# Kernel optimization log

Hardware: AMD Instinct MI355X
Metric: run time of the kernel (lower is better)

Reference implementation:

```python
import jax, jax.numpy as jnp
import numpy as np

SEQ_LEN, N_FEAT, EMB = 512, 8, 64
HID = 2 * EMB  # 128
BATCH = 512


def _lstm_layer(x, Wih, Whh, bih, bhh):
    """Single-layer LSTM, batch_first x: [B,T,F]. PyTorch gate order i,f,g,o.
    Returns (outputs [B,T,H], final hidden [B,H])."""
    B = x.shape[0]
    H = Whh.shape[1]
    # precompute input projections for all timesteps: [B,T,4H]
    xp = jnp.einsum('btf,gf->btg', x, Wih) + bih + bhh

    def step(carry, xt):
        h, c = carry
        gates = xt + h @ Whh.T  # [B,4H]
        i, f, g, o = jnp.split(gates, 4, axis=-1)
        i = jax.nn.sigmoid(i)
        f = jax.nn.sigmoid(f)
        g = jnp.tanh(g)
        o = jax.nn.sigmoid(o)
        c = f * c + i * g
        h = o * jnp.tanh(c)
        return (h, c), h

    h0 = jnp.zeros((B, H), dtype=x.dtype)
    c0 = jnp.zeros((B, H), dtype=x.dtype)
    (hT, _), hs = jax.lax.scan(step, (h0, c0), xp.transpose(1, 0, 2))
    return hs.transpose(1, 0, 2), hT


def setup_inputs() -> dict:
    key = jax.random.key(0)
    ks = jax.random.split(key, 13)
    inp = {"x": jax.random.normal(ks[0], (BATCH, SEQ_LEN, N_FEAT), dtype=jnp.float32)}

    def mk(k, shape, fan):
        s = 1.0 / np.sqrt(fan)
        return jax.random.uniform(k, shape, dtype=jnp.float32, minval=-s, maxval=s)

    # layer 1: in=N_FEAT, hid=HID
    inp["Wih1"] = mk(ks[1], (4 * HID, N_FEAT), HID)
    inp["Whh1"] = mk(ks[2], (4 * HID, HID), HID)
    inp["bih1"] = mk(ks[3], (4 * HID,), HID)
    inp["bhh1"] = mk(ks[4], (4 * HID,), HID)
    # layer 2: in=HID, hid=HID
    inp["Wih2"] = mk(ks[5], (4 * HID, HID), HID)
    inp["Whh2"] = mk(ks[6], (4 * HID, HID), HID)
    inp["bih2"] = mk(ks[7], (4 * HID,), HID)
    inp["bhh2"] = mk(ks[8], (4 * HID,), HID)
    # layer 3: in=HID, hid=EMB
    inp["Wih3"] = mk(ks[9], (4 * EMB, HID), EMB)
    inp["Whh3"] = mk(ks[10], (4 * EMB, EMB), EMB)
    inp["bih3"] = mk(ks[11], (4 * EMB,), EMB)
    inp["bhh3"] = mk(ks[12], (4 * EMB,), EMB)
    return inp


def reference(x, Wih1, Whh1, bih1, bhh1, Wih2, Whh2, bih2, bhh2, Wih3, Whh3, bih3, bhh3):
    B = x.shape[0]
    x = x.reshape(B, SEQ_LEN, N_FEAT)
    x, _ = _lstm_layer(x, Wih1, Whh1, bih1, bhh1)
    x, _ = _lstm_layer(x, Wih2, Whh2, bih2, bhh2)
    _, hT = _lstm_layer(x, Wih3, Whh3, bih3, bhh3)
    return hT  # [B, EMB]
```

## Files before the change

### kernel.cpp

```cpp
#include <hip/hip_runtime.h>


#define DEVI __device__ __forceinline__

typedef _Float16 h4 __attribute__((ext_vector_type(4)));
typedef _Float16 h8 __attribute__((ext_vector_type(8)));
typedef float f4 __attribute__((ext_vector_type(4)));

static constexpr int T_ = 512, TC_ = 16, NC_ = T_ / TC_, RC_ = 2;

DEVI float rcpf_(float x) { return __builtin_amdgcn_rcpf(x); }
DEVI float exp2f_(float x) { return __builtin_amdgcn_exp2f(x); }

DEVI h8 cvt8(const float* p) {
    const float4 a = *reinterpret_cast<const float4*>(p);
    const float4 b = *reinterpret_cast<const float4*>(p + 4);
    return h8{(_Float16)a.x, (_Float16)a.y, (_Float16)a.z, (_Float16)a.w,
              (_Float16)b.x, (_Float16)b.y, (_Float16)b.z, (_Float16)b.w};
}

DEVI void lds_barrier() {
    asm volatile("s_waitcnt lgkmcnt(0)\n\ts_barrier" ::: "memory");
}
DEVI int ld_flag(int* f) {
    return __hip_atomic_load(f, __ATOMIC_RELAXED, __HIP_MEMORY_SCOPE_AGENT);
}
DEVI void st_flag(int* f, int v) {
    __hip_atomic_store(f, v, __ATOMIC_RELAXED, __HIP_MEMORY_SCOPE_AGENT);
}

#define POINTWISE_PROLOG(ACC)                                                   \
    float e0[4], e1[4], e2[4], e3[4];                                           \
    _Pragma("unroll") for (int i = 0; i < 4; i++) {                             \
        e0[i] = exp2f_(ACC[0][i] * -1.44269504f);                               \
        e1[i] = exp2f_(ACC[1][i] * -1.44269504f);                               \
        e2[i] = exp2f_(ACC[2][i] * -2.88539008f);                               \
        e3[i] = exp2f_(ACC[3][i] * -1.44269504f); }

#define POINTWISE_CELL(i, C, HVAR)                                              \
    const float gi = rcpf_(1.f + e0[i]), gf = rcpf_(1.f + e1[i]);               \
    const float gg = 2.f * rcpf_(1.f + e2[i]) - 1.f, go = rcpf_(1.f + e3[i]);   \
    C[i] = gf * C[i] + gi * gg;                                                 \
    const float HVAR = go * (2.f * rcpf_(1.f + exp2f_(C[i] * -2.88539008f)) - 1.f);

DEVI void stage_L1(int tile, char* smem, const float* x, const float* Wih,
                   const float* Whh, const float* bih, const float* bhh,
                   _Float16* o1, int* c1, int* p1) {
    constexpr int H = 128, KT_H = 4, HP = H + 8;
    const int tid = threadIdx.x, lane = tid & 63, wv = tid >> 6;
    const int lr = lane & 15, lk = lane >> 4;
    const int b0 = tile * 16;
    const int jcol = wv * 16 + lr;
    _Float16 (*h_lds)[16][HP] = (_Float16 (*)[16][HP])smem;

    h8 wbh[4][KT_H], wbx[4];
    float bias[4];
#pragma unroll
    for (int q = 0; q < 4; q++) {
#pragma unroll
        for (int kt = 0; kt < KT_H; kt++)
            wbh[q][kt] = cvt8(Whh + (size_t)(q * H + jcol) * H + kt * 32 + lk * 8);
        wbx[q] = (lk == 0) ? cvt8(Wih + (size_t)(q * H + jcol) * 8) : h8{};
        bias[q] = bih[q * H + jcol] + bhh[q * H + jcol];
    }
    float c[4] = {0.f, 0.f, 0.f, 0.f};
    for (int i = tid; i < 2 * 16 * HP; i += 512) ((_Float16*)smem)[i] = (_Float16)0;
    __syncthreads();

    auto load_x = [&](int t, h8& xa) {
        xa = (lk == 0) ? cvt8(x + ((size_t)(b0 + lr) * T_ + t) * 8) : h8{};
    };
    h8 xa, xb;

#define L1_STEP(TT, CUR, XS) {                                                  \
    const int tt = (TT);                                                        \
    h8 ha[KT_H];                                                                \
    _Pragma("unroll") for (int kt = 0; kt < KT_H; kt++)                         \
        ha[kt] = *reinterpret_cast<const h8*>(&h_lds[CUR][lr][kt * 32 + lk * 8]); \
    f4 acc[4];                                                                  \
    _Pragma("unroll") for (int q = 0; q < 4; q++)                               \
        acc[q] = f4{bias[q], bias[q], bias[q], bias[q]};                        \
    _Pragma("unroll") for (int q = 0; q < 4; q++)                               \
        acc[q] = __builtin_amdgcn_mfma_f32_16x16x32_f16(XS, wbx[q], acc[q], 0, 0, 0); \
    _Pragma("unroll") for (int kt = 0; kt < KT_H; kt++)                         \
        _Pragma("unroll") for (int q = 0; q < 4; q++)                           \
            acc[q] = __builtin_amdgcn_mfma_f32_16x16x32_f16(ha[kt], wbh[q][kt], acc[q], 0, 0, 0); \
    if (tt + 2 < TC_) load_x(t0 + tt + 2, XS);                                  \
    POINTWISE_PROLOG(acc)                                                       \
    _Pragma("unroll") for (int i = 0; i < 4; i++) {                             \
        POINTWISE_CELL(i, c, h)                                                 \
        const int row = lk * 4 + i;                                             \
        h_lds[(CUR) ^ 1][row][jcol] = (_Float16)h;                              \
        o1[(((size_t)(tile * RC_ + slot) * TC_ + tt) * 16 + row) * 128 + jcol] = (_Float16)h; } }

    for (int ch = 0; ch < NC_; ch++) {
        const int slot = ch & (RC_ - 1);
        if (tid == 0) {
            while (ld_flag(c1) < ch - (RC_ - 1)) __builtin_amdgcn_s_sleep(8);
        }
        __syncthreads();
        const int t0 = ch * TC_;
        load_x(t0, xa); load_x(t0 + 1, xb);
        for (int tb = 0; tb < TC_ / 2; tb++) {
            L1_STEP(2 * tb, 0, xa) lds_barrier();
            L1_STEP(2 * tb + 1, 1, xb) lds_barrier();
        }
        asm volatile("s_waitcnt vmcnt(0)" ::: "memory");
        __syncthreads();
        if (tid == 0) { __threadfence(); st_flag(p1, ch + 1); }
    }
#undef L1_STEP
}

DEVI void stage_P2(int tile, const _Float16* o1, _Float16* xp, const float* Wih,
                   const float* bih, const float* bhh,
                   int* p1, int* c1, int* cx, int* px) {
    constexpr int H = 128;
    const int tid = threadIdx.x, lane = tid & 63, wv = tid >> 6;
    const int lr = lane & 15, lk = lane >> 4;
    const int jcol = wv * 16 + lr;

    h8 wbx[4][4];
    float pbias[4];
#pragma unroll
    for (int q = 0; q < 4; q++) {
#pragma unroll
        for (int kt = 0; kt < 4; kt++)
            wbx[q][kt] = cvt8(Wih + (size_t)(q * H + jcol) * 128 + kt * 32 + lk * 8);
        pbias[q] = bih[q * H + jcol] + bhh[q * H + jcol];
    }

    for (int ch = 0; ch < NC_; ch++) {
        const int slot = ch & (RC_ - 1);
        if (tid == 0) {
            while (ld_flag(p1) < ch + 1) __builtin_amdgcn_s_sleep(8);
            while (ld_flag(cx) < ch - (RC_ - 1)) __builtin_amdgcn_s_sleep(8);
            __threadfence();
        }
        __syncthreads();
        const size_t ib = (size_t)(tile * RC_ + slot) * TC_ * 2048;
        const size_t ob = (size_t)(tile * RC_ + slot) * TC_ * 8192;
#pragma unroll 4
        for (int t = 0; t < TC_; t++) {
            h8 af[4];
#pragma unroll
            for (int kt = 0; kt < 4; kt++)
                af[kt] = *reinterpret_cast<const h8*>(o1 + ib + (size_t)t * 2048 + lr * 128 + kt * 32 + lk * 8);
            f4 acc[4];
#pragma unroll
            for (int q = 0; q < 4; q++) acc[q] = f4{pbias[q], pbias[q], pbias[q], pbias[q]};
#pragma unroll
            for (int kt = 0; kt < 4; kt++)
#pragma unroll
                for (int q = 0; q < 4; q++)
                    acc[q] = __builtin_amdgcn_mfma_f32_16x16x32_f16(af[kt], wbx[q][kt], acc[q], 0, 0, 0);
#pragma unroll
            for (int q = 0; q < 4; q++) {
                const h4 o = h4{(_Float16)acc[q][0], (_Float16)acc[q][1],
                                (_Float16)acc[q][2], (_Float16)acc[q][3]};
                *reinterpret_cast<h4*>(xp + ob + (size_t)t * 8192 + (wv * 4 + q) * 256 + lane * 4) = o;
            }
        }
        asm volatile("s_waitcnt vmcnt(0)" ::: "memory");
        __syncthreads();
        if (tid == 0) { __threadfence(); st_flag(px, ch + 1); st_flag(c1, ch + 1); }
    }
}

DEVI void stage_L2(int tile, char* smem, const _Float16* xp, _Float16* O2,
                   const float* Whh, int* px, int* cx, int* p2) {
    constexpr int H = 128, KT_H = 4, HP = H + 8;
    const int tid = threadIdx.x, lane = tid & 63, wv = tid >> 6;
    const int lr = lane & 15, lk = lane >> 4;
    const int b0 = tile * 16;
    const int jcol = wv * 16 + lr;
    _Float16 (*h_lds)[16][HP] = (_Float16 (*)[16][HP])smem;

    h8 wbh[4][KT_H];
#pragma unroll
    for (int q = 0; q < 4; q++)
#pragma unroll
        for (int kt = 0; kt < KT_H; kt++)
            wbh[q][kt] = cvt8(Whh + (size_t)(q * H + jcol) * H + kt * 32 + lk * 8);

    float c[4] = {0.f, 0.f, 0.f, 0.f};
    for (int i = tid; i < 2 * 16 * HP; i += 512) ((_Float16*)smem)[i] = (_Float16)0;
    __syncthreads();

    h4 xqa[4], xqb[4];

#define LOAD_XP(SLOT, TTL, DST) {                                               \
    const size_t base = ((size_t)(tile * RC_ + (SLOT)) * TC_ + (TTL)) * 8192 + wv * 1024 + lane * 4; \
    _Pragma("unroll") for (int q = 0; q < 4; q++)                               \
        DST[q] = *reinterpret_cast<const h4*>(xp + base + q * 256); }

#define L2_STEP(TT, CUR, XQ) {                                                  \
    const int tt = (TT); const int t = t0 + tt;                                 \
    h8 ha[KT_H];                                                                \
    _Pragma("unroll") for (int kt = 0; kt < KT_H; kt++)                         \
        ha[kt] = *reinterpret_cast<const h8*>(&h_lds[CUR][lr][kt * 32 + lk * 8]); \
    f4 acc[4];                                                                  \
    _Pragma("unroll") for (int q = 0; q < 4; q++)                               \
        acc[q] = f4{(float)XQ[q][0], (float)XQ[q][1], (float)XQ[q][2], (float)XQ[q][3]}; \
    _Pragma("unroll") for (int kt = 0; kt < KT_H; kt++)                         \
        _Pragma("unroll") for (int q = 0; q < 4; q++)                           \
            acc[q] = __builtin_amdgcn_mfma_f32_16x16x32_f16(ha[kt], wbh[q][kt], acc[q], 0, 0, 0); \
    if (tt + 2 < TC_) LOAD_XP(slot, tt + 2, XQ)                                 \
    POINTWISE_PROLOG(acc)                                                       \
    _Pragma("unroll") for (int i = 0; i < 4; i++) {                             \
        POINTWISE_CELL(i, c, h)                                                 \
        const int row = lk * 4 + i;                                             \
        h_lds[(CUR) ^ 1][row][jcol] = (_Float16)h;                              \
        O2[((size_t)(b0 + row) * T_ + t) * 128 + jcol] = (_Float16)h; } }

    for (int ch = 0; ch < NC_; ch++) {
        const int slot = ch & (RC_ - 1);
        if (tid == 0) {
            while (ld_flag(px) < ch + 1) __builtin_amdgcn_s_sleep(8);
            __threadfence();
        }
        __syncthreads();
        const int t0 = ch * TC_;
        LOAD_XP(slot, 0, xqa)
        LOAD_XP(slot, 1, xqb)
        for (int tb = 0; tb < TC_ / 2; tb++) {
            L2_STEP(2 * tb, 0, xqa) lds_barrier();
            L2_STEP(2 * tb + 1, 1, xqb) lds_barrier();
        }
        asm volatile("s_waitcnt vmcnt(0)" ::: "memory");
        __syncthreads();
        if (tid == 0) { __threadfence(); st_flag(p2, ch + 1); st_flag(cx, ch + 1); }
    }
#undef L2_STEP
#undef LOAD_XP
}

DEVI void stage_L3(int tile, char* smem, const _Float16* O2, const float* Wih,
                   const float* Whh, const float* bih, const float* bhh,
                   float* out, int* p2) {
    constexpr int H = 64, KT_H = 2, KT_X = 4, HP = H + 8;
    const int tid = threadIdx.x, lane = tid & 63, wv = tid >> 6;
    const int lr = lane & 15, lk = lane >> 4;
    const int b0 = tile * 16;
    const bool act = (wv < 4);
    const int jcol = (wv & 3) * 16 + lr;
    _Float16 (*h_lds)[16][HP] = (_Float16 (*)[16][HP])smem;

    h8 wbh[4][KT_H], wbx[4][KT_X];
    float bias[4];
    if (act) {
#pragma unroll
        for (int q = 0; q < 4; q++) {
#pragma unroll
            for (int kt = 0; kt < KT_H; kt++)
                wbh[q][kt] = cvt8(Whh + (size_t)(q * H + jcol) * H + kt * 32 + lk * 8);
#pragma unroll
            for (int kt = 0; kt < KT_X; kt++)
                wbx[q][kt] = cvt8(Wih + (size_t)(q * H + jcol) * 128 + kt * 32 + lk * 8);
            bias[q] = bih[q * H + jcol] + bhh[q * H + jcol];
        }
    }
    float c[4] = {0.f, 0.f, 0.f, 0.f};
    for (int i = tid; i < 2 * 16 * HP; i += 512) ((_Float16*)smem)[i] = (_Float16)0;
    __syncthreads();

    auto load_x = [&](int t, h8* xa) {
#pragma unroll
        for (int kt = 0; kt < KT_X; kt++)
            xa[kt] = *reinterpret_cast<const h8*>(
                O2 + ((size_t)(b0 + lr) * T_ + t) * 128 + kt * 32 + lk * 8);
    };
    h8 xa[KT_X], xb[KT_X];

#define L3_STEP(TT, CUR, XS) {                                                  \
    const int tt = (TT); const int t = t0 + tt;                                 \
    if (act) {                                                                  \
        h8 ha[KT_H];                                                            \
        _Pragma("unroll") for (int kt = 0; kt < KT_H; kt++)                     \
            ha[kt] = *reinterpret_cast<const h8*>(&h_lds[CUR][lr][kt * 32 + lk * 8]); \
        f4 acc[4];                                                              \
        _Pragma("unroll") for (int q = 0; q < 4; q++)                           \
            acc[q] = f4{bias[q], bias[q], bias[q], bias[q]};                    \
        _Pragma("unroll") for (int kt = 0; kt < KT_X; kt++)                     \
            _Pragma("unroll") for (int q = 0; q < 4; q++)                       \
                acc[q] = __builtin_amdgcn_mfma_f32_16x16x32_f16(XS[kt], wbx[q][kt], acc[q], 0, 0, 0); \
        _Pragma("unroll") for (int kt = 0; kt < KT_H; kt++)                     \
            _Pragma("unroll") for (int q = 0; q < 4; q++)                       \
                acc[q] = __builtin_amdgcn_mfma_f32_16x16x32_f16(ha[kt], wbh[q][kt], acc[q], 0, 0, 0); \
        if (tt + 2 < TC_) load_x(t + 2, XS);                                    \
        POINTWISE_PROLOG(acc)                                                   \
        _Pragma("unroll") for (int i = 0; i < 4; i++) {                         \
            POINTWISE_CELL(i, c, h)                                             \
            const int row = lk * 4 + i;                                         \
            h_lds[(CUR) ^ 1][row][jcol] = (_Float16)h;                          \
            if (t == T_ - 1) out[(size_t)(b0 + row) * 64 + jcol] = h; } } }

    for (int ch = 0; ch < NC_; ch++) {
        if (tid == 0) {
            while (ld_flag(p2) < ch + 1) __builtin_amdgcn_s_sleep(8);
            __threadfence();
        }
        __syncthreads();
        const int t0 = ch * TC_;
        if (act) { load_x(t0, xa); load_x(t0 + 1, xb); }
        for (int tb = 0; tb < TC_ / 2; tb++) {
            L3_STEP(2 * tb, 0, xa) lds_barrier();
            L3_STEP(2 * tb + 1, 1, xb) lds_barrier();
        }
    }
#undef L3_STEP
}

__global__ __launch_bounds__(512, 1)
void mega_k(const float* __restrict__ x,
            const float* __restrict__ Wih1, const float* __restrict__ Whh1,
            const float* __restrict__ bih1, const float* __restrict__ bhh1,
            const float* __restrict__ Wih2, const float* __restrict__ Whh2,
            const float* __restrict__ bih2, const float* __restrict__ bhh2,
            const float* __restrict__ Wih3, const float* __restrict__ Whh3,
            const float* __restrict__ bih3, const float* __restrict__ bhh3,
            _Float16* __restrict__ o1ring, _Float16* __restrict__ xpring,
            _Float16* __restrict__ O2, float* __restrict__ out,
            int* __restrict__ flags) {
    extern __shared__ char smem[];
    const int bid = blockIdx.x;
    int* p1 = flags;
    int* c1 = flags + 32;
    int* px = flags + 64;
    int* cx = flags + 96;
    int* p2 = flags + 128;
    if (bid < 32) {
        stage_L1(bid, smem, x, Wih1, Whh1, bih1, bhh1, o1ring, c1 + bid, p1 + bid);
    } else if (bid < 64) {
        const int t = bid - 32;
        stage_P2(t, o1ring, xpring, Wih2, bih2, bhh2, p1 + t, c1 + t, cx + t, px + t);
    } else if (bid < 96) {
        const int t = bid - 64;
        stage_L2(t, smem, xpring, O2, Whh2, px + t, cx + t, p2 + t);
    } else {
        const int t = bid - 96;
        stage_L3(t, smem, O2, Wih3, Whh3, bih3, bhh3, out, p2 + t);
    }
}

__global__ void zero_flags_k(int* flags) {
    if (threadIdx.x < 160)
        __hip_atomic_store(flags + threadIdx.x, 0, __ATOMIC_RELAXED,
                           __HIP_MEMORY_SCOPE_AGENT);
}

extern "C" void kernel_launch(void* const* d_in, const int* in_sizes, int n_in,
                              void* d_out, int out_size, void* d_ws, size_t ws_size,
                              hipStream_t stream) {
    const float* x = (const float*)d_in[0];
    float* out = (float*)d_out;

    char* ws = (char*)d_ws;
    _Float16* o1ring = (_Float16*)ws;
    _Float16* xpring = (_Float16*)(ws + (size_t)4194304);
    _Float16* O2     = (_Float16*)(ws + (size_t)20971520);
    int* flags       = (int*)(ws + (size_t)88080384);
    (void)ws_size; (void)in_sizes; (void)n_in; (void)out_size;

    zero_flags_k<<<1, 192, 0, stream>>>(flags);
    mega_k<<<128, 512, 8704, stream>>>(
        x,
        (const float*)d_in[1], (const float*)d_in[2], (const float*)d_in[3], (const float*)d_in[4],
        (const float*)d_in[5], (const float*)d_in[6], (const float*)d_in[7], (const float*)d_in[8],
        (const float*)d_in[9], (const float*)d_in[10], (const float*)d_in[11], (const float*)d_in[12],
        o1ring, xpring, O2, out, flags);
}
```

Measured before the change: 711.4 us.

## Fold activation exponent scales into weights, deepen ring buffers, make O2 time-major

Pre-multiplies the weights and biases of each gate by the -log2(e) or -2log2(e) factor when they are converted to fp16. This removes the per-element multiply before exp2 in the recurrent pointwise step. The ring depth goes from 2 to 4 chunks, so the producer and consumer stages can run further apart, and the layer-2 output buffer is stored time-major so each timestep's slab is contiguous. Scaling before fp16 rounding changes numerics slightly and raises the magnitude of the fp16 weights, and the larger rings increase the workspace footprint.

Result: no change. 712.2 us (+0.1%).

```diff
diff --git a/kernel.cpp b/kernel.cpp
--- a/kernel.cpp
+++ b/kernel.cpp
@@ -7,16 +7,18 @@
 typedef _Float16 h8 __attribute__((ext_vector_type(8)));
 typedef float f4 __attribute__((ext_vector_type(4)));
 
-static constexpr int T_ = 512, TC_ = 16, NC_ = T_ / TC_, RC_ = 2;
+static constexpr int T_ = 512, TC_ = 16, NC_ = T_ / TC_, RC_ = 4;
+static constexpr float KS_ = -1.44269504f;
+static constexpr float KG_ = -2.88539008f;
 
 DEVI float rcpf_(float x) { return __builtin_amdgcn_rcpf(x); }
 DEVI float exp2f_(float x) { return __builtin_amdgcn_exp2f(x); }
 
-DEVI h8 cvt8(const float* p) {
+DEVI h8 cvt8s(const float* p, float s) {
     const float4 a = *reinterpret_cast<const float4*>(p);
     const float4 b = *reinterpret_cast<const float4*>(p + 4);
-    return h8{(_Float16)a.x, (_Float16)a.y, (_Float16)a.z, (_Float16)a.w,
-              (_Float16)b.x, (_Float16)b.y, (_Float16)b.z, (_Float16)b.w};
+    return h8{(_Float16)(a.x * s), (_Float16)(a.y * s), (_Float16)(a.z * s), (_Float16)(a.w * s),
+              (_Float16)(b.x * s), (_Float16)(b.y * s), (_Float16)(b.z * s), (_Float16)(b.w * s)};
 }
 
 DEVI void lds_barrier() {
@@ -32,16 +34,18 @@
 #define POINTWISE_PROLOG(ACC)                                                   \
     float e0[4], e1[4], e2[4], e3[4];                                           \
     _Pragma("unroll") for (int i = 0; i < 4; i++) {                             \
-        e0[i] = exp2f_(ACC[0][i] * -1.44269504f);                               \
-        e1[i] = exp2f_(ACC[1][i] * -1.44269504f);                               \
-        e2[i] = exp2f_(ACC[2][i] * -2.88539008f);                               \
-        e3[i] = exp2f_(ACC[3][i] * -1.44269504f); }
+        e0[i] = exp2f_(ACC[0][i]);                                              \
+        e1[i] = exp2f_(ACC[1][i]);                                              \
+        e2[i] = exp2f_(ACC[2][i]);                                              \
+        e3[i] = exp2f_(ACC[3][i]); }
 
 #define POINTWISE_CELL(i, C, HVAR)                                              \
     const float gi = rcpf_(1.f + e0[i]), gf = rcpf_(1.f + e1[i]);               \
     const float gg = 2.f * rcpf_(1.f + e2[i]) - 1.f, go = rcpf_(1.f + e3[i]);   \
     C[i] = gf * C[i] + gi * gg;                                                 \
-    const float HVAR = go * (2.f * rcpf_(1.f + exp2f_(C[i] * -2.88539008f)) - 1.f);
+    const float HVAR = go * (2.f * rcpf_(1.f + exp2f_(C[i] * KG_)) - 1.f);
+
+DEVI float gscale(int q) { return (q == 2) ? KG_ : KS_; }
 
 DEVI void stage_L1(int tile, char* smem, const float* x, const float* Wih,
                    const float* Whh, const float* bih, const float* bhh,
@@ -57,20 +61,21 @@
     float bias[4];
 #pragma unroll
     for (int q = 0; q < 4; q++) {
+        const float s = gscale(q);
 #pragma unroll
         for (int kt = 0; kt < KT_H; kt++)
-            wbh[q][kt] = cvt8(Whh + (size_t)(q * H + jcol) * H + kt * 32 + lk * 8);
-        wbx[q] = (lk == 0) ? cvt8(Wih + (size_t)(q * H + jcol) * 8) : h8{};
-        bias[q] = bih[q * H + jcol] + bhh[q * H + jcol];
+            wbh[q][kt] = cvt8s(Whh + (size_t)(q * H + jcol) * H + kt * 32 + lk * 8, s);
+        wbx[q] = (lk == 0) ? cvt8s(Wih + (size_t)(q * H + jcol) * 8, s) : h8{};
+        bias[q] = (bih[q * H + jcol] + bhh[q * H + jcol]) * s;
     }
     float c[4] = {0.f, 0.f, 0.f, 0.f};
     for (int i = tid; i < 2 * 16 * HP; i += 512) ((_Float16*)smem)[i] = (_Float16)0;
     __syncthreads();
 
     auto load_x = [&](int t, h8& xa) {
-        xa = (lk == 0) ? cvt8(x + ((size_t)(b0 + lr) * T_ + t) * 8) : h8{};
+        if (lk == 0) xa = cvt8s(x + ((size_t)(b0 + lr) * T_ + t) * 8, 1.f);
     };
-    h8 xa, xb;
+    h8 xa = h8{}, xb = h8{};
 
 #define L1_STEP(TT, CUR, XS) {                                                  \
     const int tt = (TT);                                                        \
@@ -124,10 +129,11 @@
     float pbias[4];
 #pragma unroll
     for (int q = 0; q < 4; q++) {
+        const float s = gscale(q);
 #pragma unroll
         for (int kt = 0; kt < 4; kt++)
-            wbx[q][kt] = cvt8(Wih + (size_t)(q * H + jcol) * 128 + kt * 32 + lk * 8);
-        pbias[q] = bih[q * H + jcol] + bhh[q * H + jcol];
+            wbx[q][kt] = cvt8s(Wih + (size_t)(q * H + jcol) * 128 + kt * 32 + lk * 8, s);
+        pbias[q] = (bih[q * H + jcol] + bhh[q * H + jcol]) * s;
     }
 
     for (int ch = 0; ch < NC_; ch++) {
@@ -178,11 +184,12 @@
 
     h8 wbh[4][KT_H];
 #pragma unroll
-    for (int q = 0; q < 4; q++)
+    for (int q = 0; q < 4; q++) {
+        const float s = gscale(q);
 #pragma unroll
         for (int kt = 0; kt < KT_H; kt++)
-            wbh[q][kt] = cvt8(Whh + (size_t)(q * H + jcol) * H + kt * 32 + lk * 8);
-
+            wbh[q][kt] = cvt8s(Whh + (size_t)(q * H + jcol) * H + kt * 32 + lk * 8, s);
+    }
     float c[4] = {0.f, 0.f, 0.f, 0.f};
     for (int i = tid; i < 2 * 16 * HP; i += 512) ((_Float16*)smem)[i] = (_Float16)0;
     __syncthreads();
@@ -211,7 +218,7 @@
         POINTWISE_CELL(i, c, h)                                                 \
         const int row = lk * 4 + i;                                             \
         h_lds[(CUR) ^ 1][row][jcol] = (_Float16)h;                              \
-        O2[((size_t)(b0 + row) * T_ + t) * 128 + jcol] = (_Float16)h; } }
+        O2[((size_t)t * 512 + (b0 + row)) * 128 + jcol] = (_Float16)h; } }
 
     for (int ch = 0; ch < NC_; ch++) {
         const int slot = ch & (RC_ - 1);
@@ -251,13 +258,14 @@
     if (act) {
 #pragma unroll
         for (int q = 0; q < 4; q++) {
+            const float s = gscale(q);
 #pragma unroll
             for (int kt = 0; kt < KT_H; kt++)
-                wbh[q][kt] = cvt8(Whh + (size_t)(q * H + jcol) * H + kt * 32 + lk * 8);
+                wbh[q][kt] = cvt8s(Whh + (size_t)(q * H + jcol) * H + kt * 32 + lk * 8, s);
 #pragma unroll
             for (int kt = 0; kt < KT_X; kt++)
-                wbx[q][kt] = cvt8(Wih + (size_t)(q * H + jcol) * 128 + kt * 32 + lk * 8);
-            bias[q] = bih[q * H + jcol] + bhh[q * H + jcol];
+                wbx[q][kt] = cvt8s(Wih + (size_t)(q * H + jcol) * 128 + kt * 32 + lk * 8, s);
+            bias[q] = (bih[q * H + jcol] + bhh[q * H + jcol]) * s;
         }
     }
     float c[4] = {0.f, 0.f, 0.f, 0.f};
@@ -268,7 +276,7 @@
 #pragma unroll
         for (int kt = 0; kt < KT_X; kt++)
             xa[kt] = *reinterpret_cast<const h8*>(
-                O2 + ((size_t)(b0 + lr) * T_ + t) * 128 + kt * 32 + lk * 8);
+                O2 + ((size_t)t * 512 + (b0 + lr)) * 128 + kt * 32 + lk * 8);
     };
     h8 xa[KT_X], xb[KT_X];
 
@@ -357,9 +365,9 @@
 
     char* ws = (char*)d_ws;
     _Float16* o1ring = (_Float16*)ws;
-    _Float16* xpring = (_Float16*)(ws + (size_t)4194304);
-    _Float16* O2     = (_Float16*)(ws + (size_t)20971520);
-    int* flags       = (int*)(ws + (size_t)88080384);
+    _Float16* xpring = (_Float16*)(ws + (size_t)8388608);
+    _Float16* O2     = (_Float16*)(ws + (size_t)41943040);
+    int* flags       = (int*)(ws + (size_t)109051904);
     (void)ws_size; (void)in_sizes; (void)n_in; (void)out_size;
 
     zero_flags_k<<<1, 192, 0, stream>>>(flags);
```
